# Kernel tuning notes

Measured on AMD Instinct MI355X. Metric: run time of the kernel, lower is better.

## Reference

```python
import jax, jax.numpy as jnp
import numpy as np


def setup_inputs() -> dict:
    key = jax.random.key(0)
    k1, k2 = jax.random.split(key)
    N = 33554432
    x = jax.random.normal(k1, (N,), dtype=jnp.float32)
    y = jax.random.randint(k2, (N,), 0, 2, dtype=jnp.int32)
    return {"x": x, "y": y}


def reference(x, y):
    # normalize x to [0, 1]
    xmin = jnp.min(x)
    xmax = jnp.max(x) - xmin
    xn = ((x - xmin) / xmax).reshape(-1)
    # grouped means by binary label
    m0 = (y == 0)
    n0 = jnp.sum(m0).astype(xn.dtype)
    n1 = xn.shape[0] - n0
    s0 = jnp.sum(jnp.where(m0, xn, 0.0))
    s1 = jnp.sum(xn) - s0
    lbas = s0 / n0
    lhaut = s1 / n1
    # swap so lbas <= lhaut, then difference (always <= 0)
    l = jnp.minimum(lbas, lhaut) - jnp.maximum(lbas, lhaut)
    return l.reshape(1)
```

## Files before the change

kernel.cpp:

```cpp
#include <hip/hip_runtime.h>
#include <math.h>

#define NB1 2048
#define BS 256
#define LQ 4
#define NBATCH 4
#define P2BS 512

typedef float __attribute__((ext_vector_type(4))) vfloat4;
typedef int   __attribute__((ext_vector_type(4))) vint4;

__device__ __forceinline__ void ld_nt_f4(const vfloat4* p, vfloat4& d) {
    asm volatile("global_load_dwordx4 %0, %1, off nt" : "=v"(d) : "v"(p));
}
__device__ __forceinline__ void ld_nt_i4(const vint4* p, vint4& d) {
    asm volatile("global_load_dwordx4 %0, %1, off nt" : "=v"(d) : "v"(p));
}

#define ISSUE(R0, R1, R2, R3, W0, W1, W2, W3, t)                    \
    do {                                                            \
        const vfloat4* _px = x4 + base0 + (t) * (LQ * BS);          \
        const vint4*   _py = y4 + base0 + (t) * (LQ * BS);          \
        ld_nt_f4(_px + 0 * BS, R0);                                 \
        ld_nt_f4(_px + 1 * BS, R1);                                 \
        ld_nt_f4(_px + 2 * BS, R2);                                 \
        ld_nt_f4(_px + 3 * BS, R3);                                 \
        ld_nt_i4(_py + 0 * BS, W0);                                 \
        ld_nt_i4(_py + 1 * BS, W1);                                 \
        ld_nt_i4(_py + 2 * BS, W2);                                 \
        ld_nt_i4(_py + 3 * BS, W3);                                 \
    } while (0)

#define WAIT_PREV(R0, R1, R2, R3, W0, W1, W2, W3)                   \
    asm volatile("s_waitcnt vmcnt(8)"                               \
                 : "+v"(R0), "+v"(R1), "+v"(R2), "+v"(R3),          \
                   "+v"(W0), "+v"(W1), "+v"(W2), "+v"(W3))

#define WAIT_LAST(R0, R1, R2, R3, W0, W1, W2, W3)                   \
    asm volatile("s_waitcnt vmcnt(0)"                               \
                 : "+v"(R0), "+v"(R1), "+v"(R2), "+v"(R3),          \
                   "+v"(W0), "+v"(W1), "+v"(W2), "+v"(W3))

__device__ __forceinline__ void consume(vfloat4 v0, vfloat4 v1, vfloat4 v2, vfloat4 v3,
                                        vint4 w0, vint4 w1, vint4 w2, vint4 w3,
                                        double& sum, double& sum0, int& cnt0,
                                        float& mn, float& mx) {
    float fs[LQ], ft[LQ], fmn[LQ], fmx[LQ];
    int   fc[LQ];
    const vfloat4 vv[LQ] = {v0, v1, v2, v3};
    const vint4   ww[LQ] = {w0, w1, w2, w3};
    #pragma unroll
    for (int q = 0; q < LQ; ++q) {
        vfloat4 v = vv[q];
        vint4   w = ww[q];
        fs[q] = (v.x + v.y) + (v.z + v.w);
        float a  = (w.x == 0) ? v.x : 0.0f;
        float b  = (w.y == 0) ? v.y : 0.0f;
        float cc = (w.z == 0) ? v.z : 0.0f;
        float d  = (w.w == 0) ? v.w : 0.0f;
        ft[q] = (a + b) + (cc + d);
        fc[q] = (w.x == 0) + (w.y == 0) + (w.z == 0) + (w.w == 0);
        fmn[q] = fminf(fminf(v.x, v.y), fminf(v.z, v.w));
        fmx[q] = fmaxf(fmaxf(v.x, v.y), fmaxf(v.z, v.w));
    }
    float sA = (fs[0] + fs[1]) + (fs[2] + fs[3]);
    float tA = (ft[0] + ft[1]) + (ft[2] + ft[3]);
    sum  += (double)sA;
    sum0 += (double)tA;
    cnt0 += (fc[0] + fc[1]) + (fc[2] + fc[3]);
    mn = fminf(mn, fminf(fminf(fmn[0], fmn[1]), fminf(fmn[2], fmn[3])));
    mx = fmaxf(mx, fmaxf(fmaxf(fmx[0], fmx[1]), fmaxf(fmx[2], fmx[3])));
}


__global__ __launch_bounds__(BS) void risk_pass1(const float* __restrict__ x,
                                                 const int* __restrict__ y,
                                                 double* __restrict__ ws) {
    const vfloat4* __restrict__ x4 = (const vfloat4*)x;
    const vint4*   __restrict__ y4 = (const vint4*)y;

    const int base0 = blockIdx.x * (NBATCH * LQ * BS) + threadIdx.x;

    vfloat4 a0, a1, a2, a3;  vint4 b0, b1, b2, b3;
    vfloat4 c0, c1, c2, c3;  vint4 d0, d1, d2, d3;

    double sum = 0.0, sum0 = 0.0;
    int    cnt0 = 0;
    float  mn =  INFINITY, mx = -INFINITY;

    ISSUE(a0, a1, a2, a3, b0, b1, b2, b3, 0);

    ISSUE(c0, c1, c2, c3, d0, d1, d2, d3, 1);
    WAIT_PREV(a0, a1, a2, a3, b0, b1, b2, b3);
    consume(a0, a1, a2, a3, b0, b1, b2, b3, sum, sum0, cnt0, mn, mx);

    ISSUE(a0, a1, a2, a3, b0, b1, b2, b3, 2);
    WAIT_PREV(c0, c1, c2, c3, d0, d1, d2, d3);
    consume(c0, c1, c2, c3, d0, d1, d2, d3, sum, sum0, cnt0, mn, mx);

    ISSUE(c0, c1, c2, c3, d0, d1, d2, d3, 3);
    WAIT_PREV(a0, a1, a2, a3, b0, b1, b2, b3);
    consume(a0, a1, a2, a3, b0, b1, b2, b3, sum, sum0, cnt0, mn, mx);

    WAIT_LAST(c0, c1, c2, c3, d0, d1, d2, d3);
    consume(c0, c1, c2, c3, d0, d1, d2, d3, sum, sum0, cnt0, mn, mx);

    for (int off = 32; off > 0; off >>= 1) {
        sum  += __shfl_down(sum,  off);
        sum0 += __shfl_down(sum0, off);
        cnt0 += __shfl_down(cnt0, off);
        mn = fminf(mn, __shfl_down(mn, off));
        mx = fmaxf(mx, __shfl_down(mx, off));
    }

    __shared__ double s_sum[BS / 64], s_sum0[BS / 64];
    __shared__ int    s_cnt[BS / 64];
    __shared__ float  s_mn[BS / 64], s_mx[BS / 64];

    int lane = threadIdx.x & 63;
    int wave = threadIdx.x >> 6;
    if (lane == 0) {
        s_sum[wave] = sum; s_sum0[wave] = sum0; s_cnt[wave] = cnt0;
        s_mn[wave] = mn; s_mx[wave] = mx;
    }
    __syncthreads();

    if (threadIdx.x == 0) {
        double bsum = s_sum[0], bsum0 = s_sum0[0];
        int bcnt = s_cnt[0];
        float bmn = s_mn[0], bmx = s_mx[0];
        #pragma unroll
        for (int w = 1; w < BS / 64; ++w) {
            bsum += s_sum[w]; bsum0 += s_sum0[w]; bcnt += s_cnt[w];
            bmn = fminf(bmn, s_mn[w]); bmx = fmaxf(bmx, s_mx[w]);
        }
        ws[0 * NB1 + blockIdx.x] = bsum;
        ws[1 * NB1 + blockIdx.x] = bsum0;
        ws[2 * NB1 + blockIdx.x] = (double)bcnt;
        ws[3 * NB1 + blockIdx.x] = (double)bmn;
        ws[4 * NB1 + blockIdx.x] = (double)bmx;
    }
}

__global__ __launch_bounds__(P2BS) void risk_pass2(const double* __restrict__ ws,
                                                   float* __restrict__ out,
                                                   long long n_total) {
    double sum = 0.0, sum0 = 0.0, cnt0 = 0.0;
    double mn =  INFINITY;
    double mx = -INFINITY;

    for (int i = threadIdx.x; i < NB1; i += P2BS) {
        sum  += ws[0 * NB1 + i];
        sum0 += ws[1 * NB1 + i];
        cnt0 += ws[2 * NB1 + i];
        mn = fmin(mn, ws[3 * NB1 + i]);
        mx = fmax(mx, ws[4 * NB1 + i]);
    }

    for (int off = 32; off > 0; off >>= 1) {
        sum  += __shfl_down(sum,  off);
        sum0 += __shfl_down(sum0, off);
        cnt0 += __shfl_down(cnt0, off);
        mn = fmin(mn, __shfl_down(mn, off));
        mx = fmax(mx, __shfl_down(mx, off));
    }

    __shared__ double s_sum[P2BS / 64], s_sum0[P2BS / 64], s_cnt[P2BS / 64];
    __shared__ double s_mn[P2BS / 64], s_mx[P2BS / 64];
    int lane = threadIdx.x & 63;
    int wave = threadIdx.x >> 6;
    if (lane == 0) {
        s_sum[wave] = sum; s_sum0[wave] = sum0; s_cnt[wave] = cnt0;
        s_mn[wave] = mn; s_mx[wave] = mx;
    }
    __syncthreads();

    if (threadIdx.x == 0) {
        double tsum = s_sum[0], tsum0 = s_sum0[0], tcnt0 = s_cnt[0];
        double tmn = s_mn[0], tmx = s_mx[0];
        #pragma unroll
        for (int w = 1; w < P2BS / 64; ++w) {
            tsum += s_sum[w]; tsum0 += s_sum0[w]; tcnt0 += s_cnt[w];
            tmn = fmin(tmn, s_mn[w]); tmx = fmax(tmx, s_mx[w]);
        }
        double range = tmx - tmn;
        double n1 = (double)n_total - tcnt0;
        double sum1 = tsum - tsum0;
        double m0 = (tsum0 / tcnt0 - tmn) / range;
        double m1 = (sum1  / n1    - tmn) / range;
        double l = fmin(m0, m1) - fmax(m0, m1);
        out[0] = (float)l;
    }
}

extern "C" void kernel_launch(void* const* d_in, const int* in_sizes, int n_in,
                              void* d_out, int out_size, void* d_ws, size_t ws_size,
                              hipStream_t stream) {
    const float* x = (const float*)d_in[0];
    const int*   y = (const int*)d_in[1];
    float* out = (float*)d_out;
    double* ws = (double*)d_ws;
    long long n = (long long)in_sizes[0];

    risk_pass1<<<NB1, BS, 0, stream>>>(x, y, ws);
    risk_pass2<<<1, P2BS, 0, stream>>>(ws, out, n);
}
```

Baseline: 251.5 us.

## Stage pass-1 loads through LDS with global_load_lds double buffering

Replaces the register-based nontemporal vector loads in the first reduction pass with direct global-to-LDS loads (global_load_lds) into a double-buffered shared-memory tile, followed by a per-batch barrier and LDS reads. The aim is to keep more bytes in flight without spending VGPRs on staging registers. In exchange it adds block-wide barriers every batch, extra LDS traffic, and drops the nontemporal hint. Per-block work stays the same (8 batches of 512 float4).

```diff
diff --git a/kernel.cpp b/kernel.cpp
--- a/kernel.cpp
+++ b/kernel.cpp
@@ -3,74 +3,17 @@
 
 #define NB1 2048
 #define BS 256
-#define LQ 4
-#define NBATCH 4
+#define NBATCH 8
+#define F4B 512
+#define F4_PER_BLOCK (NBATCH * F4B)
 #define P2BS 512
 
 typedef float __attribute__((ext_vector_type(4))) vfloat4;
 typedef int   __attribute__((ext_vector_type(4))) vint4;
 
-__device__ __forceinline__ void ld_nt_f4(const vfloat4* p, vfloat4& d) {
-    asm volatile("global_load_dwordx4 %0, %1, off nt" : "=v"(d) : "v"(p));
-}
-__device__ __forceinline__ void ld_nt_i4(const vint4* p, vint4& d) {
-    asm volatile("global_load_dwordx4 %0, %1, off nt" : "=v"(d) : "v"(p));
-}
-
-#define ISSUE(R0, R1, R2, R3, W0, W1, W2, W3, t)                    \
-    do {                                                            \
-        const vfloat4* _px = x4 + base0 + (t) * (LQ * BS);          \
-        const vint4*   _py = y4 + base0 + (t) * (LQ * BS);          \
-        ld_nt_f4(_px + 0 * BS, R0);                                 \
-        ld_nt_f4(_px + 1 * BS, R1);                                 \
-        ld_nt_f4(_px + 2 * BS, R2);                                 \
-        ld_nt_f4(_px + 3 * BS, R3);                                 \
-        ld_nt_i4(_py + 0 * BS, W0);                                 \
-        ld_nt_i4(_py + 1 * BS, W1);                                 \
-        ld_nt_i4(_py + 2 * BS, W2);                                 \
-        ld_nt_i4(_py + 3 * BS, W3);                                 \
-    } while (0)
-
-#define WAIT_PREV(R0, R1, R2, R3, W0, W1, W2, W3)                   \
-    asm volatile("s_waitcnt vmcnt(8)"                               \
-                 : "+v"(R0), "+v"(R1), "+v"(R2), "+v"(R3),          \
-                   "+v"(W0), "+v"(W1), "+v"(W2), "+v"(W3))
-
-#define WAIT_LAST(R0, R1, R2, R3, W0, W1, W2, W3)                   \
-    asm volatile("s_waitcnt vmcnt(0)"                               \
-                 : "+v"(R0), "+v"(R1), "+v"(R2), "+v"(R3),          \
-                   "+v"(W0), "+v"(W1), "+v"(W2), "+v"(W3))
-
-__device__ __forceinline__ void consume(vfloat4 v0, vfloat4 v1, vfloat4 v2, vfloat4 v3,
-                                        vint4 w0, vint4 w1, vint4 w2, vint4 w3,
-                                        double& sum, double& sum0, int& cnt0,
-                                        float& mn, float& mx) {
-    float fs[LQ], ft[LQ], fmn[LQ], fmx[LQ];
-    int   fc[LQ];
-    const vfloat4 vv[LQ] = {v0, v1, v2, v3};
-    const vint4   ww[LQ] = {w0, w1, w2, w3};
-    #pragma unroll
-    for (int q = 0; q < LQ; ++q) {
-        vfloat4 v = vv[q];
-        vint4   w = ww[q];
-        fs[q] = (v.x + v.y) + (v.z + v.w);
-        float a  = (w.x == 0) ? v.x : 0.0f;
-        float b  = (w.y == 0) ? v.y : 0.0f;
-        float cc = (w.z == 0) ? v.z : 0.0f;
-        float d  = (w.w == 0) ? v.w : 0.0f;
-        ft[q] = (a + b) + (cc + d);
-        fc[q] = (w.x == 0) + (w.y == 0) + (w.z == 0) + (w.w == 0);
-        fmn[q] = fminf(fminf(v.x, v.y), fminf(v.z, v.w));
-        fmx[q] = fmaxf(fmaxf(v.x, v.y), fmaxf(v.z, v.w));
-    }
-    float sA = (fs[0] + fs[1]) + (fs[2] + fs[3]);
-    float tA = (ft[0] + ft[1]) + (ft[2] + ft[3]);
-    sum  += (double)sA;
-    sum0 += (double)tA;
-    cnt0 += (fc[0] + fc[1]) + (fc[2] + fc[3]);
-    mn = fminf(mn, fminf(fminf(fmn[0], fmn[1]), fminf(fmn[2], fmn[3])));
-    mx = fmaxf(mx, fmaxf(fmaxf(fmx[0], fmx[1]), fmaxf(fmx[2], fmx[3])));
-}
+typedef const __attribute__((address_space(1))) void GAS;
+typedef __attribute__((address_space(3))) void LAS;
+#define GLDS(g, l) __builtin_amdgcn_global_load_lds((GAS*)(g), (LAS*)(l), 16, 0, 0)
 
 
 __global__ __launch_bounds__(BS) void risk_pass1(const float* __restrict__ x,
@@ -79,31 +22,73 @@
     const vfloat4* __restrict__ x4 = (const vfloat4*)x;
     const vint4*   __restrict__ y4 = (const vint4*)y;
 
-    const int base0 = blockIdx.x * (NBATCH * LQ * BS) + threadIdx.x;
+    __shared__ vfloat4 lx[2][F4B];
+    __shared__ vint4   ly[2][F4B];
 
-    vfloat4 a0, a1, a2, a3;  vint4 b0, b1, b2, b3;
-    vfloat4 c0, c1, c2, c3;  vint4 d0, d1, d2, d3;
+    const int t    = threadIdx.x;
+    const int w64  = t & ~63;
+    const int gchunk = blockIdx.x * F4_PER_BLOCK;
 
     double sum = 0.0, sum0 = 0.0;
     int    cnt0 = 0;
     float  mn =  INFINITY, mx = -INFINITY;
 
-    ISSUE(a0, a1, a2, a3, b0, b1, b2, b3, 0);
+    auto stage = [&](int b, int buf) {
+        const int g = gchunk + b * F4B;
+        GLDS(&x4[g + t],        &lx[buf][w64]);
+        GLDS(&x4[g + 256 + t],  &lx[buf][256 + w64]);
+        GLDS(&y4[g + t],        &ly[buf][w64]);
+        GLDS(&y4[g + 256 + t],  &ly[buf][256 + w64]);
+    };
 
-    ISSUE(c0, c1, c2, c3, d0, d1, d2, d3, 1);
-    WAIT_PREV(a0, a1, a2, a3, b0, b1, b2, b3);
-    consume(a0, a1, a2, a3, b0, b1, b2, b3, sum, sum0, cnt0, mn, mx);
+    stage(0, 0);
 
-    ISSUE(a0, a1, a2, a3, b0, b1, b2, b3, 2);
-    WAIT_PREV(c0, c1, c2, c3, d0, d1, d2, d3);
-    consume(c0, c1, c2, c3, d0, d1, d2, d3, sum, sum0, cnt0, mn, mx);
+    #pragma unroll 2
+    for (int b = 0; b < NBATCH; ++b) {
+        const int buf = b & 1;
+        if (b + 1 < NBATCH) {
+            stage(b + 1, buf ^ 1);
+            asm volatile("s_waitcnt vmcnt(4)" ::: "memory");
+        } else {
+            asm volatile("s_waitcnt vmcnt(0)" ::: "memory");
+        }
+        __builtin_amdgcn_sched_barrier(0);
+        __builtin_amdgcn_s_barrier();
+        asm volatile("" ::: "memory");
 
-    ISSUE(c0, c1, c2, c3, d0, d1, d2, d3, 3);
-    WAIT_PREV(a0, a1, a2, a3, b0, b1, b2, b3);
-    consume(a0, a1, a2, a3, b0, b1, b2, b3, sum, sum0, cnt0, mn, mx);
+        vfloat4 v0 = lx[buf][t];
+        vfloat4 v1 = lx[buf][256 + t];
+        vint4   u0 = ly[buf][t];
+        vint4   u1 = ly[buf][256 + t];
 
-    WAIT_LAST(c0, c1, c2, c3, d0, d1, d2, d3);
-    consume(c0, c1, c2, c3, d0, d1, d2, d3, sum, sum0, cnt0, mn, mx);
+        float s0 = (v0.x + v0.y) + (v0.z + v0.w);
+        float s1 = (v1.x + v1.y) + (v1.z + v1.w);
+        float a0 = (u0.x == 0) ? v0.x : 0.0f;
+        float b0_ = (u0.y == 0) ? v0.y : 0.0f;
+        float c0 = (u0.z == 0) ? v0.z : 0.0f;
+        float d0 = (u0.w == 0) ? v0.w : 0.0f;
+        float a1 = (u1.x == 0) ? v1.x : 0.0f;
+        float b1_ = (u1.y == 0) ? v1.y : 0.0f;
+        float c1 = (u1.z == 0) ? v1.z : 0.0f;
+        float d1 = (u1.w == 0) ? v1.w : 0.0f;
+        float t0 = (a0 + b0_) + (c0 + d0);
+        float t1 = (a1 + b1_) + (c1 + d1);
+        int   c  = (u0.x == 0) + (u0.y == 0) + (u0.z == 0) + (u0.w == 0)
+                 + (u1.x == 0) + (u1.y == 0) + (u1.z == 0) + (u1.w == 0);
+        float bmn = fminf(fminf(fminf(v0.x, v0.y), fminf(v0.z, v0.w)),
+                          fminf(fminf(v1.x, v1.y), fminf(v1.z, v1.w)));
+        float bmx = fmaxf(fmaxf(fmaxf(v0.x, v0.y), fmaxf(v0.z, v0.w)),
+                          fmaxf(fmaxf(v1.x, v1.y), fmaxf(v1.z, v1.w)));
+
+        sum  += (double)(s0 + s1);
+        sum0 += (double)(t0 + t1);
+        cnt0 += c;
+        mn = fminf(mn, bmn);
+        mx = fmaxf(mx, bmx);
+
+        asm volatile("" ::: "memory");
+        __builtin_amdgcn_s_barrier();
+    }
 
     for (int off = 32; off > 0; off >>= 1) {
         sum  += __shfl_down(sum,  off);
```

After: 284.6 us. 1.13x slower.
